# Kernel optimization log

Measured on AMD Instinct MI355X. Metric: run time of the kernel, lower is better.

## Reference

```python
import jax, jax.numpy as jnp
import numpy as np

N, E, F, HID, HEADS, L, B, R = 50000, 400000, 64, 256, 4, 4, 16, 8
C = HID // HEADS  # per-head channels = 64
LN_EPS = 1e-5
NEG_SLOPE = 0.2  # GATConv LeakyReLU default


def _posenc(n, d):
    pos = jnp.arange(n, dtype=jnp.float32)[:, None]
    i = jnp.arange(d, dtype=jnp.float32)[None, :]
    rates = 1.0 / 10000.0 ** (2.0 * jnp.floor(i / 2.0) / d)
    ang = pos * rates
    return jnp.where(jnp.arange(d)[None, :] % 2 == 0, jnp.sin(ang), jnp.cos(ang))


def _layernorm(x, g, b):
    mu = x.mean(-1, keepdims=True)
    var = ((x - mu) ** 2).mean(-1, keepdims=True)
    return (x - mu) * jax.lax.rsqrt(var + LN_EPS) * g + b


def _gat_layer(x, src, dst, W, a_src, a_dst, bias):
    # x: [N, HID]; W: [HID, HID]; a_src/a_dst: [HEADS, C]; bias: [HID]
    h = (x @ W).reshape(N, HEADS, C)
    s_src = (h * a_src[None]).sum(-1)  # [N, HEADS]
    s_dst = (h * a_dst[None]).sum(-1)  # [N, HEADS]
    e = jax.nn.leaky_relu(s_src[src] + s_dst[dst], NEG_SLOPE)  # [E', HEADS]
    m = jax.ops.segment_max(e, dst, num_segments=N)
    ex = jnp.exp(e - m[dst])
    denom = jax.ops.segment_sum(ex, dst, num_segments=N)
    alpha = ex / denom[dst]  # softmax over incoming edges per dst node
    out = jax.ops.segment_sum(alpha[:, :, None] * h[src], dst, num_segments=N)
    return out.reshape(N, HID) + bias


def setup_inputs() -> dict:
    key = jax.random.key(0)
    ks = jax.random.split(key, 20)
    sc = 0.05
    batch = jnp.sort(jax.random.randint(ks[2], (N,), 0, B))
    return {
        "x": jax.random.normal(ks[0], (N, F), jnp.float32),
        "region_emb_w": jax.random.normal(ks[3], (R, F), jnp.float32) * sc,
        "in_proj_w": jax.random.normal(ks[4], (3 * F, HID), jnp.float32) * sc,
        "in_proj_b": jnp.zeros((HID,), jnp.float32),
        "gat_w": jax.random.normal(ks[5], (L, HID, HID), jnp.float32) * sc,
        "att_src": jax.random.normal(ks[6], (L, HEADS, C), jnp.float32) * sc,
        "att_dst": jax.random.normal(ks[7], (L, HEADS, C), jnp.float32) * sc,
        "gat_b": jnp.zeros((L, HID), jnp.float32),
        "ln_g": jnp.ones((L, HID), jnp.float32),
        "ln_b": jnp.zeros((L, HID), jnp.float32),
        "ro_w1": jax.random.normal(ks[8], (HID, HID), jnp.float32) * sc,
        "ro_b1": jnp.zeros((HID,), jnp.float32),
        "ro_w2": jax.random.normal(ks[9], (HID, HID), jnp.float32) * sc,
        "ro_b2": jnp.zeros((HID,), jnp.float32),
        "edge_index": jax.random.randint(ks[1], (2, E), 0, N),
        "batch": batch,
        "region_ids": jax.random.randint(ks[10], (N,), 0, R),
    }


def reference(x, region_emb_w, in_proj_w, in_proj_b, gat_w, att_src, att_dst,
              gat_b, ln_g, ln_b, ro_w1, ro_b1, ro_w2, ro_b2,
              edge_index, batch, region_ids):
    # input features: x | region embedding | sinusoidal posenc  -> [N, 3F]
    feats = jnp.concatenate([x, region_emb_w[region_ids], _posenc(N, F)], axis=-1)
    h = feats @ in_proj_w + in_proj_b
    # add self loops once (GATConv add_self_loops=True)
    loop = jnp.arange(N)
    src = jnp.concatenate([edge_index[0], loop])
    dst = jnp.concatenate([edge_index[1], loop])
    for l in range(L):
        h = _gat_layer(h, src, dst, gat_w[l], att_src[l], att_dst[l], gat_b[l])
        h = _layernorm(jax.nn.relu(h), ln_g[l], ln_b[l])
        # dropout is identity in eval mode
    # global mean pool over graphs
    sums = jax.ops.segment_sum(h, batch, num_segments=B)
    cnts = jax.ops.segment_sum(jnp.ones((N,), h.dtype), batch, num_segments=B)
    pooled = sums / jnp.maximum(cnts, 1.0)[:, None]  # [B, HID]
    out = jax.nn.gelu(pooled @ ro_w1 + ro_b1, approximate=False) @ ro_w2 + ro_b2
    return out
```

## Files before the change

### kernel.cpp

```cpp
#include <hip/hip_runtime.h>
#include <cmath>

typedef unsigned short u16;
typedef unsigned char u8;
typedef unsigned int u32;
typedef short bf16x8 __attribute__((ext_vector_type(8)));
typedef float f32x4 __attribute__((ext_vector_type(4)));
typedef float f32x2 __attribute__((ext_vector_type(2)));

#define NN 50000
#define MP 50048
#define EE 400000
#define ET 450000
#define HIDD 256
#define KIN 192
#define LN_EPSF 1e-5f

__device__ __forceinline__ float bf2f(u16 u){ return __uint_as_float(((u32)u)<<16); }
__device__ __forceinline__ u16 f2bf(float f){
  u32 x = __float_as_uint(f);
  u32 r = x + 0x7fffu + ((x>>16)&1u);
  return (u16)(r>>16);
}
__device__ __forceinline__ u32 pack2(float a, float b){ return (u32)f2bf(a) | ((u32)f2bf(b)<<16); }
__device__ __forceinline__ u8 f2fp8(float v){
  return (u8)(__builtin_amdgcn_cvt_pk_fp8_f32(v, v, 0, false) & 0xff);
}

__device__ __forceinline__ void dma16(const u16* g, u16* lds){
  __builtin_amdgcn_global_load_lds(
      (const __attribute__((address_space(1))) void*)g,
      (__attribute__((address_space(3))) void*)lds, 16, 0, 0);
}

__global__ __launch_bounds__(256) void k_setup(
    const float* __restrict__ x, const float* __restrict__ remb, const int* __restrict__ rid,
    u16* __restrict__ feats,
    const float* __restrict__ ipw, const float* __restrict__ gatw,
    u16* __restrict__ wtin, u16* __restrict__ wtl,
    const float* __restrict__ asrc, const float* __restrict__ adst, u16* __restrict__ vmat,
    const int* __restrict__ ei, int* __restrict__ deg,
    const float* __restrict__ ipb, u16* __restrict__ vmatc, float* __restrict__ bias0)
{
  int b = blockIdx.x;
  if (b < 1564){
    int u = b*256 + threadIdx.x;
    int n = u >> 3;
    int c0 = (u & 7) * 8;
    uint4 o = {0u,0u,0u,0u};
    if (n < NN){
      const float* xp = x + (size_t)n*64 + c0;
      float4 v0 = *(const float4*)xp;
      float4 v1 = *(const float4*)(xp + 4);
      o.x = pack2(v0.x, v0.y); o.y = pack2(v0.z, v0.w);
      o.z = pack2(v1.x, v1.y); o.w = pack2(v1.z, v1.w);
    }
    *(uint4*)(feats + (size_t)n*192 + c0) = o;
  } else if (b < 3128){
    int u = (b-1564)*256 + threadIdx.x;
    int n = u >> 3;
    int c0 = (u & 7) * 8;
    uint4 o = {0u,0u,0u,0u};
    if (n < NN){
      const float* rp = remb + (size_t)rid[n]*64 + c0;
      float4 v0 = *(const float4*)rp;
      float4 v1 = *(const float4*)(rp + 4);
      o.x = pack2(v0.x, v0.y); o.y = pack2(v0.z, v0.w);
      o.z = pack2(v1.x, v1.y); o.w = pack2(v1.z, v1.w);
    }
    *(uint4*)(feats + (size_t)n*192 + 64 + c0) = o;
  } else if (b < 4692){
    int u = (b-3128)*256 + threadIdx.x;
    int n = u >> 3;
    int i0 = (u & 7) * 8;
    uint4 o = {0u,0u,0u,0u};
    if (n < NN){
      float fn = (float)n;
      float os[8];
      #pragma unroll
      for (int m=0;m<4;++m){
        float rate = exp2f(-(float)(i0 + 2*m) * (1.0f/64.0f) * 13.287712379549449f);
        float s, c;
        __sincosf(fn * rate, &s, &c);
        os[2*m] = s; os[2*m+1] = c;
      }
      o.x = pack2(os[0], os[1]); o.y = pack2(os[2], os[3]);
      o.z = pack2(os[4], os[5]); o.w = pack2(os[6], os[7]);
    }
    *(uint4*)(feats + (size_t)n*192 + 128 + i0) = o;
  } else if (b < 5908){
    int idx = (b - 4692)*256 + threadIdx.x;
    if (idx < 49152){
      int k = idx >> 8, n = idx & 255;
      const float* wrow = ipw + (size_t)k*256;
      float s = 0.f;
      #pragma unroll 8
      for (int j=0;j<256;++j) s += wrow[j] * gatw[(size_t)j*256 + n];
      wtin[n*192 + k] = f2bf(s);
    } else {
      int j = idx - 49152;
      if (j < 262144){
        int l = j >> 16, rem = j & 65535;
        int n = rem >> 8, k = rem & 255;
        wtl[j] = f2bf(gatw[l*65536 + k*256 + n]);
      }
    }
  } else if (b < 5972){
    int idx = (b - 5908)*256 + threadIdx.x;
    if (idx < 16384){
      int l = idx >> 12, rem = idx & 4095, v = rem >> 8, k = rem & 255;
      float s = 0.f;
      if (v < 8){
        const float* a = (v < 4) ? (asrc + l*256 + v*64) : (adst + l*256 + (v-4)*64);
        const float* w = gatw + (size_t)l*65536 + k*256 + (v & 3)*64;
        #pragma unroll 8
        for (int c=0;c<64;++c) s += w[c]*a[c];
      }
      vmat[idx] = f2bf(s);
    }
  } else if (b < 5980){
    int v = b - 5972;
    __shared__ float w0a[256];
    int t = threadIdx.x;
    {
      const float* a = (v < 4) ? (asrc + v*64) : (adst + (v-4)*64);
      const float* w = gatw + (size_t)t*256 + (v & 3)*64;
      float s = 0.f;
      #pragma unroll 8
      for (int c=0;c<64;++c) s += w[c]*a[c];
      w0a[t] = s;
    }
    __syncthreads();
    if (t < 192){
      const float* wrow = ipw + (size_t)t*256;
      float s = 0.f;
      #pragma unroll 8
      for (int j=0;j<256;++j) s += wrow[j]*w0a[j];
      vmatc[v*192 + t] = f2bf(s);
      vmatc[(v+8)*192 + t] = 0;
    }
  } else if (b < 5981){
    int t = threadIdx.x;
    __shared__ float c0[256];
    {
      float s = 0.f;
      for (int k=0;k<256;++k) s += ipb[k] * gatw[(size_t)k*256 + t];
      c0[t] = s;
      bias0[t] = s;
    }
    __syncthreads();
    if (t < 8){
      const float* a = (t < 4) ? (asrc + t*64) : (adst + (t-4)*64);
      float s = 0.f;
      for (int c=0;c<64;++c) s += c0[(t & 3)*64 + c] * a[c];
      bias0[256 + t] = s;
    }
  } else {
    int i = (b - 5981)*256 + threadIdx.x;
    if (i < ET){
      int d = (i < EE) ? ei[EE + i] : (i - EE);
      atomicAdd(&deg[d], 1);
    }
  }
}

__global__ void k_scan1(const int* __restrict__ deg, int* __restrict__ row_off, int* __restrict__ part){
  __shared__ int s[256];
  int n = blockIdx.x*256 + threadIdx.x;
  int v = (n < NN) ? deg[n] : 0;
  s[threadIdx.x] = v;
  __syncthreads();
  for (int off=1; off<256; off<<=1){
    int t = (threadIdx.x >= off) ? s[threadIdx.x - off] : 0;
    __syncthreads();
    s[threadIdx.x] += t;
    __syncthreads();
  }
  if (n < NN) row_off[n] = s[threadIdx.x] - v;
  if (threadIdx.x == 255) part[blockIdx.x] = s[255];
}

__global__ void k_scan23(int* __restrict__ row_off, const int* __restrict__ part, int nparts){
  __shared__ int sp[256];
  int t = threadIdx.x;
  sp[t] = (t < nparts && t < (int)blockIdx.x) ? part[t] : 0;
  __syncthreads();
  for (int off=128; off; off>>=1){
    if (t < off) sp[t] += sp[t+off];
    __syncthreads();
  }
  int n = blockIdx.x*256 + t;
  if (n < NN) row_off[n] += sp[0];
}

__global__ void k_scatter(const int* __restrict__ ei, const int* __restrict__ row_off,
                          int* __restrict__ cur, int* __restrict__ csr_src){
  int i = blockIdx.x*blockDim.x + threadIdx.x;
  if (i >= ET) return;
  int s, d;
  if (i < EE){ s = ei[i]; d = ei[EE + i]; } else { s = i - EE; d = i - EE; }
  int pos = row_off[d] + atomicAdd(&cur[d], 1);
  csr_src[pos] = s;
}

template<int K>
__global__ __launch_bounds__(256, 3) void k_gemm(
    const u16* __restrict__ A, const u16* __restrict__ Wt,
    const float* __restrict__ bias, const u16* __restrict__ vmat,
    const float* __restrict__ sbias,
    float* __restrict__ ss, float* __restrict__ sd,
    u16* __restrict__ C, u8* __restrict__ C8, int M)
{
  __shared__ u16 Asl[2][128*32];
  __shared__ u16 Bsl[2][128*32];
  int tid = threadIdx.x;
  int wave = tid >> 6, lane = tid & 63, quad = lane >> 4, lm = lane & 15;

  int bid0 = blockIdx.x;
  int xcd = bid0 & 7, off = bid0 >> 3;
  const int q = 782 >> 3, r = 782 & 7;
  int wgid = (xcd < r ? xcd*(q+1) : r*(q+1) + (xcd - r)*q) + off;
  int r0 = (wgid >> 1) * 128;
  int cb = wgid & 1;

  int rW = (wave >> 1) * 64;
  int cW = (wave & 1) * 64;
  bool doScore = vmat && (cb == 0) && ((wave & 1) == 0);

  f32x4 acc[4][4] = {};
  f32x4 accs[4] = {};

  auto stage = [&](int buf, int k0){
    for (int m = wave; m < 8; m += 4){
      int s = m*64 + lane;
      int rr = s >> 2, p = s & 3;
      int c = p ^ ((rr >> 2) & 3);
      dma16(A + (size_t)(r0 + rr)*K + k0 + c*8, &Asl[buf][m*512]);
    }
    for (int m = wave; m < 8; m += 4){
      int s = m*64 + lane;
      int rr = s >> 2, p = s & 3;
      int c = p ^ ((rr >> 2) & 3);
      dma16(Wt + (size_t)(cb*128 + rr)*K + k0 + c*8, &Bsl[buf][m*512]);
    }
  };

  stage(0, 0);
  __syncthreads();

  for (int ks = 0; ks < K/32; ++ks){
    int cur = ks & 1;
    if (ks + 1 < K/32) stage(cur ^ 1, (ks+1)*32);

    bf16x8 a[4], b[4];
    #pragma unroll
    for (int i=0;i<4;++i){
      int row = rW + i*16 + lm;
      int slot = row*4 + (quad ^ ((row >> 2) & 3));
      a[i] = *(const bf16x8*)(&Asl[cur][slot*8]);
    }
    #pragma unroll
    for (int j=0;j<4;++j){
      int row = cW + j*16 + lm;
      int slot = row*4 + (quad ^ ((row >> 2) & 3));
      b[j] = *(const bf16x8*)(&Bsl[cur][slot*8]);
    }
    #pragma unroll
    for (int i=0;i<4;++i)
      #pragma unroll
      for (int j=0;j<4;++j)
        acc[i][j] = __builtin_amdgcn_mfma_f32_16x16x32_bf16(a[i], b[j], acc[i][j], 0, 0, 0);
    if (doScore){
      bf16x8 bs = *(const bf16x8*)(vmat + (size_t)lm*K + ks*32 + quad*8);
      #pragma unroll
      for (int i=0;i<4;++i)
        accs[i] = __builtin_amdgcn_mfma_f32_16x16x32_bf16(a[i], bs, accs[i], 0, 0, 0);
    }
    __syncthreads();
  }

  if (doScore){
    float sb = sbias ? sbias[lm & 7] : 0.f;
    #pragma unroll
    for (int i=0;i<4;++i){
      #pragma unroll
      for (int r2=0;r2<4;++r2){
        int row = r0 + rW + i*16 + quad*4 + r2;
        if (row < M){
          float sv = accs[i][r2] + sb;
          if (lm < 4)      ss[row*4 + lm]     = sv;
          else if (lm < 8) sd[row*4 + lm - 4] = sv;
        }
      }
    }
  }

  #pragma unroll
  for (int i=0;i<4;++i){
    #pragma unroll
    for (int r2=0;r2<4;++r2){
      int row = r0 + rW + i*16 + quad*4 + r2;
      if (row < M){
        #pragma unroll
        for (int j=0;j<4;++j){
          int col = cb*128 + cW + j*16 + lm;
          float v = acc[i][j][r2];
          if (bias) v += bias[col];
          if (C)  C[(size_t)row*256 + col] = f2bf(v);
          if (C8) C8[(size_t)row*256 + col] = f2fp8(v);
        }
      }
    }
  }
}

__global__ __launch_bounds__(256) void k_aggregate(
    const u8* __restrict__ h8, const float* __restrict__ ssrc, const float* __restrict__ sdst,
    const int* __restrict__ row_off, const int* __restrict__ deg, const int* __restrict__ csr_src,
    const float* __restrict__ bias, const float* __restrict__ g, const float* __restrict__ bb,
    u16* __restrict__ hout, u8* __restrict__ hout8)
{
  int wv = (blockIdx.x*blockDim.x + threadIdx.x) >> 6;
  int lane = threadIdx.x & 63;
  int sub = lane >> 4;
  int ql  = lane & 15;
  int n = wv*4 + sub;
  if (n >= NN) return;
  int c0 = ql*16;
  int head = ql >> 2;
  float sdh = sdst[n*4 + head];
  int ro = row_off[n];
  int dg = deg[n];
  float denA = 0.f, denB = 0.f;
  float a[16] = {};
  float b[16] = {};

  int sA = csr_src[ro];
  int sB = (1 < dg) ? csr_src[ro + 1] : 0;
  uint4 uA = *(const uint4*)(h8 + (size_t)sA*HIDD + c0);
  uint4 uB = *(const uint4*)(h8 + (size_t)sB*HIDD + c0);
  float fA = ssrc[sA*4 + head];
  float fB = ssrc[sB*4 + head];

  for (int j = 0; j < dg; j += 2){
    int nA = (j + 2 < dg) ? csr_src[ro + j + 2] : 0;
    int nB = (j + 3 < dg) ? csr_src[ro + j + 3] : 0;
    uint4 vA = *(const uint4*)(h8 + (size_t)nA*HIDD + c0);
    uint4 vB = *(const uint4*)(h8 + (size_t)nB*HIDD + c0);
    float gA = ssrc[nA*4 + head];
    float gB = ssrc[nB*4 + head];

    float eA = fA + sdh;
    eA = (eA > 0.f) ? eA : 0.2f*eA;
    float xA = __expf(eA);
    denA += xA;
    {
      f32x2 p0 = __builtin_amdgcn_cvt_pk_f32_fp8((int)uA.x, false);
      f32x2 p1 = __builtin_amdgcn_cvt_pk_f32_fp8((int)uA.x, true);
      f32x2 p2 = __builtin_amdgcn_cvt_pk_f32_fp8((int)uA.y, false);
      f32x2 p3 = __builtin_amdgcn_cvt_pk_f32_fp8((int)uA.y, true);
      f32x2 p4 = __builtin_amdgcn_cvt_pk_f32_fp8((int)uA.z, false);
      f32x2 p5 = __builtin_amdgcn_cvt_pk_f32_fp8((int)uA.z, true);
      f32x2 p6 = __builtin_amdgcn_cvt_pk_f32_fp8((int)uA.w, false);
      f32x2 p7 = __builtin_amdgcn_cvt_pk_f32_fp8((int)uA.w, true);
      a[0]+=xA*p0.x; a[1]+=xA*p0.y; a[2]+=xA*p1.x; a[3]+=xA*p1.y;
      a[4]+=xA*p2.x; a[5]+=xA*p2.y; a[6]+=xA*p3.x; a[7]+=xA*p3.y;
      a[8]+=xA*p4.x; a[9]+=xA*p4.y; a[10]+=xA*p5.x; a[11]+=xA*p5.y;
      a[12]+=xA*p6.x; a[13]+=xA*p6.y; a[14]+=xA*p7.x; a[15]+=xA*p7.y;
    }
    float eB = fB + sdh;
    eB = (eB > 0.f) ? eB : 0.2f*eB;
    float xB = (j + 1 < dg) ? __expf(eB) : 0.f;
    denB += xB;
    {
      f32x2 p0 = __builtin_amdgcn_cvt_pk_f32_fp8((int)uB.x, false);
      f32x2 p1 = __builtin_amdgcn_cvt_pk_f32_fp8((int)uB.x, true);
      f32x2 p2 = __builtin_amdgcn_cvt_pk_f32_fp8((int)uB.y, false);
      f32x2 p3 = __builtin_amdgcn_cvt_pk_f32_fp8((int)uB.y, true);
      f32x2 p4 = __builtin_amdgcn_cvt_pk_f32_fp8((int)uB.z, false);
      f32x2 p5 = __builtin_amdgcn_cvt_pk_f32_fp8((int)uB.z, true);
      f32x2 p6 = __builtin_amdgcn_cvt_pk_f32_fp8((int)uB.w, false);
      f32x2 p7 = __builtin_amdgcn_cvt_pk_f32_fp8((int)uB.w, true);
      b[0]+=xB*p0.x; b[1]+=xB*p0.y; b[2]+=xB*p1.x; b[3]+=xB*p1.y;
      b[4]+=xB*p2.x; b[5]+=xB*p2.y; b[6]+=xB*p3.x; b[7]+=xB*p3.y;
      b[8]+=xB*p4.x; b[9]+=xB*p4.y; b[10]+=xB*p5.x; b[11]+=xB*p5.y;
      b[12]+=xB*p6.x; b[13]+=xB*p6.y; b[14]+=xB*p7.x; b[15]+=xB*p7.y;
    }
    sA = nA; sB = nB; uA = vA; uB = vB; fA = gA; fB = gB;
  }

  float inv = 1.f / (denA + denB);
  float y[16];
  float4 bi[4];
  #pragma unroll
  for (int m=0;m<4;++m) bi[m] = *(const float4*)(bias + c0 + m*4);
  #pragma unroll
  for (int k=0;k<16;++k){
    float bv = ((const float*)bi)[k];
    y[k] = fmaxf((a[k]+b[k])*inv + bv, 0.f);
  }
  float sum = 0.f;
  #pragma unroll
  for (int k=0;k<16;++k) sum += y[k];
  #pragma unroll
  for (int o=8;o>=1;o>>=1) sum += __shfl_xor(sum, o);
  float mu = sum * (1.f/256.f);
  float d[16], sq = 0.f;
  #pragma unroll
  for (int k=0;k<16;++k){ d[k] = y[k]-mu; sq += d[k]*d[k]; }
  #pragma unroll
  for (int o=8;o>=1;o>>=1) sq += __shfl_xor(sq, o);
  float rs = rsqrtf(sq*(1.f/256.f) + LN_EPSF);
  float4 gv[4], qv[4];
  #pragma unroll
  for (int m=0;m<4;++m){
    gv[m] = *(const float4*)(g + c0 + m*4);
    qv[m] = *(const float4*)(bb + c0 + m*4);
  }
  float o16[16];
  #pragma unroll
  for (int k=0;k<16;++k)
    o16[k] = d[k]*rs*((const float*)gv)[k] + ((const float*)qv)[k];

  if (hout8){
    uint4 w;
    u32 w0 = (u32)__builtin_amdgcn_cvt_pk_fp8_f32(o16[0], o16[1], 0, false);
    w.x = (u32)__builtin_amdgcn_cvt_pk_fp8_f32(o16[2], o16[3], (int)w0, true);
    w0 = (u32)__builtin_amdgcn_cvt_pk_fp8_f32(o16[4], o16[5], 0, false);
    w.y = (u32)__builtin_amdgcn_cvt_pk_fp8_f32(o16[6], o16[7], (int)w0, true);
    w0 = (u32)__builtin_amdgcn_cvt_pk_fp8_f32(o16[8], o16[9], 0, false);
    w.z = (u32)__builtin_amdgcn_cvt_pk_fp8_f32(o16[10], o16[11], (int)w0, true);
    w0 = (u32)__builtin_amdgcn_cvt_pk_fp8_f32(o16[12], o16[13], 0, false);
    w.w = (u32)__builtin_amdgcn_cvt_pk_fp8_f32(o16[14], o16[15], (int)w0, true);
    *(uint4*)(hout8 + (size_t)n*HIDD + c0) = w;
  } else {
    uint4 o4a, o4b;
    o4a.x = pack2(o16[0], o16[1]);  o4a.y = pack2(o16[2], o16[3]);
    o4a.z = pack2(o16[4], o16[5]);  o4a.w = pack2(o16[6], o16[7]);
    o4b.x = pack2(o16[8], o16[9]);  o4b.y = pack2(o16[10], o16[11]);
    o4b.z = pack2(o16[12], o16[13]); o4b.w = pack2(o16[14], o16[15]);
    *(uint4*)(hout + (size_t)n*HIDD + c0) = o4a;
    *(uint4*)(hout + (size_t)n*HIDD + c0 + 8) = o4b;
  }
}

__global__ __launch_bounds__(256) void k_pool(
    const u8* __restrict__ h8, const int* __restrict__ batch,
    float* __restrict__ pooled, float* __restrict__ cnt)
{
  const int chunk = 50;
  int t = threadIdx.x;
  int n0 = blockIdx.x*chunk;
  int n1 = min(n0 + chunk, NN);
  if (n0 >= n1) return;
  float acc = 0.f;
  int curb = batch[n0];
  int runStart = n0;
  bool hi = (t & 2) != 0;
  for (int n=n0; n<n1; ++n){
    int b = batch[n];
    if (b != curb){
      atomicAdd(&pooled[curb*HIDD + t], acc);
      if (t == 0) atomicAdd(&cnt[curb], (float)(n - runStart));
      acc = 0.f; curb = b; runStart = n;
    }
    u32 w = *(const u32*)(h8 + (size_t)n*HIDD + (t & ~3));
    f32x2 p = hi ? __builtin_amdgcn_cvt_pk_f32_fp8((int)w, true)
                 : __builtin_amdgcn_cvt_pk_f32_fp8((int)w, false);
    acc += (t & 1) ? p.y : p.x;
  }
  atomicAdd(&pooled[curb*HIDD + t], acc);
  if (t == 0) atomicAdd(&cnt[curb], (float)(n1 - runStart));
}

__global__ __launch_bounds__(256) void k_readout(
    const float* __restrict__ pooled, const float* __restrict__ cnt,
    const float* __restrict__ w1, const float* __restrict__ b1,
    const float* __restrict__ w2, const float* __restrict__ b2,
    float* __restrict__ out)
{
  __shared__ float p[256], mid[256];
  int b = blockIdx.x, t = threadIdx.x;
  float c = fmaxf(cnt[b], 1.f);
  p[t] = pooled[b*HIDD + t] / c;
  __syncthreads();
  float acc = b1[t];
  for (int k=0;k<256;++k) acc += p[k]*w1[k*256+t];
  mid[t] = 0.5f*acc*(1.f + erff(acc*0.70710678118654752f));
  __syncthreads();
  float acc2 = b2[t];
  for (int k=0;k<256;++k) acc2 += mid[k]*w2[k*256+t];
  out[b*HIDD + t] = acc2;
}

extern "C" void kernel_launch(void* const* d_in, const int* in_sizes, int n_in,
                              void* d_out, int out_size, void* d_ws, size_t ws_size,
                              hipStream_t stream)
{
  const float* x    = (const float*)d_in[0];
  const float* remb = (const float*)d_in[1];
  const float* ipw  = (const float*)d_in[2];
  const float* ipb  = (const float*)d_in[3];
  const float* gatw = (const float*)d_in[4];
  const float* asrc = (const float*)d_in[5];
  const float* adst = (const float*)d_in[6];
  const float* gatb = (const float*)d_in[7];
  const float* lng  = (const float*)d_in[8];
  const float* lnb  = (const float*)d_in[9];
  const float* row1 = (const float*)d_in[10];
  const float* rob1 = (const float*)d_in[11];
  const float* row2 = (const float*)d_in[12];
  const float* rob2 = (const float*)d_in[13];
  const int* ei   = (const int*)d_in[14];
  const int* batch= (const int*)d_in[15];
  const int* rid  = (const int*)d_in[16];

  char* ws = (char*)d_ws;
  int*   deg  = (int*)  (ws + 0);
  int*   cur  = (int*)  (ws + 200192);
  float* cnt  = (float*)(ws + 400384);
  float* pool = (float*)(ws + 400640);
  int*   row  = (int*)  (ws + 417024);
  int*   part = (int*)  (ws + 617216);
  int*   csr  = (int*)  (ws + 618240);
  float* ss   = (float*)(ws + 2418432);
  float* sd   = (float*)(ws + 3219200);
  u16*   vmat = (u16*)  (ws + 4019968);
  u16*   feats= (u16*)  (ws + 4052736);
  u16*   wtin = (u16*)  (ws + 23271168);
  u16*   wtl  = (u16*)  (ws + 23369472);
  u16*   hA   = (u16*)  (ws + 23893760);
  u8*    hA8  = (u8*)   (ws + 23893760);
  u8*    hB8  = (u8*)   (ws + 49518336);
  u16*   vmatc= (u16*)  (ws + 62330624);
  float* bias0= (float*)(ws + 62336768);

  (void)hipMemsetAsync(ws, 0, 417024, stream);

  k_setup <<<7739, 256, 0, stream>>>(x, remb, rid, feats, ipw, gatw, wtin, wtl,
                                     asrc, adst, vmat, ei, deg, ipb, vmatc, bias0);
  k_scan1 <<<196, 256, 0, stream>>>(deg, row, part);
  k_scan23<<<196, 256, 0, stream>>>(row, part, 196);
  k_scatter<<<1758, 256, 0, stream>>>(ei, row, cur, csr);

  k_gemm<KIN><<<782, 256, 0, stream>>>(feats, wtin, bias0, vmatc, bias0 + 256,
                                       ss, sd, nullptr, hB8, NN);
  k_aggregate<<<3125, 256, 0, stream>>>(hB8, ss, sd, row, deg, csr,
                                        gatb + 0*HIDD, lng + 0*HIDD, lnb + 0*HIDD,
                                        hA, nullptr);

  for (int l = 1; l < 4; ++l){
    k_gemm<HIDD><<<782, 256, 0, stream>>>(hA, wtl + (size_t)l*HIDD*HIDD, nullptr,
                                          vmat + (size_t)l*16*256, nullptr,
                                          ss, sd, nullptr, hB8, NN);
    if (l < 3){
      k_aggregate<<<3125, 256, 0, stream>>>(hB8, ss, sd, row, deg, csr,
                                            gatb + l*HIDD, lng + l*HIDD, lnb + l*HIDD,
                                            hA, nullptr);
    } else {
      k_aggregate<<<3125, 256, 0, stream>>>(hB8, ss, sd, row, deg, csr,
                                            gatb + l*HIDD, lng + l*HIDD, lnb + l*HIDD,
                                            nullptr, hA8);
    }
  }

  k_pool   <<<1000, 256, 0, stream>>>(hA8, batch, pool, cnt);
  k_readout<<<16, 256, 0, stream>>>(pool, cnt, row1, rob1, row2, rob2, (float*)d_out);
}
```

Before: 438.3 us.

## Sort destination nodes by in-degree for balanced aggregation waves

Builds a degree histogram during the scan, prefix-sums it in an extra block, and writes a permutation of nodes bucketed by degree (counting sort). The aggregate kernel processes nodes in this permuted order, so the four nodes sharing a wavefront have similar degree and lanes do not sit idle waiting on the longest neighbor list. The cost is extra atomics and setup work, plus an indirection on node index that scatters output writes and loses locality in the sdst and row_off reads.

```diff
diff --git a/kernel.cpp b/kernel.cpp
--- a/kernel.cpp
+++ b/kernel.cpp
@@ -164,10 +164,12 @@
   }
 }
 
-__global__ void k_scan1(const int* __restrict__ deg, int* __restrict__ row_off, int* __restrict__ part){
+__global__ void k_scan1(const int* __restrict__ deg, int* __restrict__ row_off, int* __restrict__ part,
+                        int* __restrict__ hist){
   __shared__ int s[256];
   int n = blockIdx.x*256 + threadIdx.x;
   int v = (n < NN) ? deg[n] : 0;
+  if (n < NN) atomicAdd(&hist[v < 255 ? v : 255], 1);
   s[threadIdx.x] = v;
   __syncthreads();
   for (int off=1; off<256; off<<=1){
@@ -180,9 +182,23 @@
   if (threadIdx.x == 255) part[blockIdx.x] = s[255];
 }
 
-__global__ void k_scan23(int* __restrict__ row_off, const int* __restrict__ part, int nparts){
+__global__ void k_scan23(int* __restrict__ row_off, const int* __restrict__ part, int nparts,
+                         int* __restrict__ hist){
   __shared__ int sp[256];
   int t = threadIdx.x;
+  if ((int)blockIdx.x == nparts){
+    int v = hist[t];
+    sp[t] = v;
+    __syncthreads();
+    for (int off=1; off<256; off<<=1){
+      int u = (t >= off) ? sp[t - off] : 0;
+      __syncthreads();
+      sp[t] += u;
+      __syncthreads();
+    }
+    hist[t] = sp[t] - v;
+    return;
+  }
   sp[t] = (t < nparts && t < (int)blockIdx.x) ? part[t] : 0;
   __syncthreads();
   for (int off=128; off; off>>=1){
@@ -194,7 +210,18 @@
 }
 
 __global__ void k_scatter(const int* __restrict__ ei, const int* __restrict__ row_off,
-                          int* __restrict__ cur, int* __restrict__ csr_src){
+                          int* __restrict__ cur, int* __restrict__ csr_src,
+                          const int* __restrict__ deg, const int* __restrict__ hist,
+                          int* __restrict__ cur2, int* __restrict__ perm){
+  if (blockIdx.x >= 1758){
+    int n = (blockIdx.x - 1758)*256 + threadIdx.x;
+    if (n < NN){
+      int d = deg[n]; d = d < 255 ? d : 255;
+      int pos = hist[d] + atomicAdd(&cur2[d], 1);
+      perm[pos] = n;
+    }
+    return;
+  }
   int i = blockIdx.x*blockDim.x + threadIdx.x;
   if (i >= ET) return;
   int s, d;
@@ -317,6 +344,7 @@
 __global__ __launch_bounds__(256) void k_aggregate(
     const u8* __restrict__ h8, const float* __restrict__ ssrc, const float* __restrict__ sdst,
     const int* __restrict__ row_off, const int* __restrict__ deg, const int* __restrict__ csr_src,
+    const int* __restrict__ perm,
     const float* __restrict__ bias, const float* __restrict__ g, const float* __restrict__ bb,
     u16* __restrict__ hout, u8* __restrict__ hout8)
 {
@@ -324,8 +352,9 @@
   int lane = threadIdx.x & 63;
   int sub = lane >> 4;
   int ql  = lane & 15;
-  int n = wv*4 + sub;
-  if (n >= NN) return;
+  int gid = wv*4 + sub;
+  if (gid >= NN) return;
+  int n = perm[gid];
   int c0 = ql*16;
   int head = ql >> 2;
   float sdh = sdst[n*4 + head];
@@ -534,18 +563,22 @@
   u8*    hB8  = (u8*)   (ws + 49518336);
   u16*   vmatc= (u16*)  (ws + 62330624);
   float* bias0= (float*)(ws + 62336768);
+  int*   hist = (int*)  (ws + 62338048);
+  int*   cur2 = (int*)  (ws + 62339072);
+  int*   perm = (int*)  (ws + 62340096);
 
   (void)hipMemsetAsync(ws, 0, 417024, stream);
+  (void)hipMemsetAsync(ws + 62338048, 0, 2048, stream);
 
   k_setup <<<7739, 256, 0, stream>>>(x, remb, rid, feats, ipw, gatw, wtin, wtl,
                                      asrc, adst, vmat, ei, deg, ipb, vmatc, bias0);
-  k_scan1 <<<196, 256, 0, stream>>>(deg, row, part);
-  k_scan23<<<196, 256, 0, stream>>>(row, part, 196);
-  k_scatter<<<1758, 256, 0, stream>>>(ei, row, cur, csr);
+  k_scan1 <<<196, 256, 0, stream>>>(deg, row, part, hist);
+  k_scan23<<<197, 256, 0, stream>>>(row, part, 196, hist);
+  k_scatter<<<1954, 256, 0, stream>>>(ei, row, cur, csr, deg, hist, cur2, perm);
 
   k_gemm<KIN><<<782, 256, 0, stream>>>(feats, wtin, bias0, vmatc, bias0 + 256,
                                        ss, sd, nullptr, hB8, NN);
-  k_aggregate<<<3125, 256, 0, stream>>>(hB8, ss, sd, row, deg, csr,
+  k_aggregate<<<3125, 256, 0, stream>>>(hB8, ss, sd, row, deg, csr, perm,
                                         gatb + 0*HIDD, lng + 0*HIDD, lnb + 0*HIDD,
                                         hA, nullptr);
 
@@ -554,11 +587,11 @@
                                           vmat + (size_t)l*16*256, nullptr,
                                           ss, sd, nullptr, hB8, NN);
     if (l < 3){
-      k_aggregate<<<3125, 256, 0, stream>>>(hB8, ss, sd, row, deg, csr,
+      k_aggregate<<<3125, 256, 0, stream>>>(hB8, ss, sd, row, deg, csr, perm,
                                             gatb + l*HIDD, lng + l*HIDD, lnb + l*HIDD,
                                             hA, nullptr);
     } else {
-      k_aggregate<<<3125, 256, 0, stream>>>(hB8, ss, sd, row, deg, csr,
+      k_aggregate<<<3125, 256, 0, stream>>>(hB8, ss, sd, row, deg, csr, perm,
                                             gatb + l*HIDD, lng + l*HIDD, lnb + l*HIDD,
                                             nullptr, hA8);
     }
```

New measurement: 777.4 us. 1.77x slower.
